# Performance work log

Hardware: AMD Instinct MI355X
Metric: run time of the kernel (lower is better)

The kernel has to match this reference:

```python
import jax, jax.numpy as jnp
import numpy as np

BS, N, D, H = 2, 512, 512, 16
DD = D // H
EPS = 1e-5


def _layernorm(h, g, b):
    mu = jnp.mean(h, axis=-1, keepdims=True)
    var = jnp.mean((h - mu) ** 2, axis=-1, keepdims=True)
    return (h - mu) / jnp.sqrt(var + EPS) * g + b


def setup_inputs() -> dict:
    key = jax.random.key(0)
    ks = jax.random.split(key, 10)
    x = jax.random.normal(ks[0], (BS, N, D), dtype=jnp.float32)
    u = jax.random.uniform(ks[1], (BS, N, N), dtype=jnp.float32)
    adj = jnp.where(u > 0.3, u, 0.0)
    s = 0.02
    return {
        "x": x,
        "adj": adj,
        "W_fc": jax.random.normal(ks[2], (D, D), dtype=jnp.float32) * s,
        "b_fc": jnp.zeros((D,), dtype=jnp.float32),
        "W_fc2": jax.random.normal(ks[3], (D, D), dtype=jnp.float32) * s,
        "b_fc2": jnp.zeros((D,), dtype=jnp.float32),
        "W_val": jax.random.normal(ks[4], (D, D), dtype=jnp.float32) * s,
        "b_val": jnp.zeros((D,), dtype=jnp.float32),
        "aff": jax.random.normal(ks[5], (H, DD), dtype=jnp.float32) * s,
        "aff_bias": jnp.zeros((H,), dtype=jnp.float32),
        "ln_g": jnp.ones((D,), dtype=jnp.float32),
        "ln_b": jnp.zeros((D,), dtype=jnp.float32),
        "t": 0,
    }


def reference(x, adj, W_fc, b_fc, W_fc2, b_fc2, W_val, b_val, aff, aff_bias, ln_g, ln_b, t):
    bs, n, d = x.shape
    # projections -> [bs, H, n, dd]
    def proj(W, b):
        return (x @ W.T + b).reshape(bs, n, H, DD).transpose(0, 2, 1, 3)
    x_val = proj(W_val, b_val)
    x_aff = proj(W_fc, b_fc)
    x_aff2 = proj(W_fc2, b_fc2)
    # GAT additive scores: leaky_relu over all (i,j) pairs, then dot with aff
    v = jax.nn.leaky_relu(x_aff[:, :, :, None, :] + x_aff2[:, :, None, :, :], 0.2)  # [bs,H,n,n,dd]
    scores = jnp.einsum('bhijd,hd->bhij', v, aff) + aff_bias[None, :, None, None]
    scores = jnp.where(adj[:, None, :, :] < 1e-5, jnp.float32(-1e9), scores)
    attn = jax.nn.softmax(scores, axis=-1)  # [bs,H,n,n]
    out = jnp.einsum('bhij,bhjd->bhid', attn, x_val)  # [bs,H,n,dd]
    out = out.transpose(0, 2, 1, 3).reshape(bs, n, d)
    x_aff_flat = x_aff.transpose(0, 2, 1, 3).reshape(bs, n, d)
    h = _layernorm(x_aff_flat + out, ln_g, ln_b)
    return jax.nn.relu(h)
```

## Files before the change

kernel.cpp:

```cpp
#include <hip/hip_runtime.h>


#define NB 2
#define NN 512
#define DM 512
#define NH 16
#define DD 32
#define RLOG2E 1.4426950408889634f

typedef __attribute__((ext_vector_type(8))) short bf16x8;
typedef __attribute__((ext_vector_type(4))) float f32x4;
typedef _Float16 h2 __attribute__((ext_vector_type(2)));
typedef __fp16 fp16x2 __attribute__((ext_vector_type(2)));

__device__ __forceinline__ h2 u2h(unsigned int u) { union { unsigned int x; h2 h; } c; c.x = u; return c.h; }
__device__ __forceinline__ unsigned int h2u(h2 v) { union { unsigned int x; h2 h; } c; c.h = v; return c.x; }
__device__ __forceinline__ h2 pkrtz(float x, float y) {
  union { fp16x2 a; h2 b; } c; c.a = __builtin_amdgcn_cvt_pkrtz(x, y); return c.b;
}

#if __has_builtin(__builtin_amdgcn_fdot2)
#define DOT2(a, b, c) __builtin_amdgcn_fdot2((a), (b), (c), false)
#else
#define DOT2(a, b, c) fmaf((float)(a)[0], (float)(b)[0], fmaf((float)(a)[1], (float)(b)[1], (c)))
#endif
#if __has_builtin(__builtin_elementwise_fma)
#define PKFMA(a, b, c) __builtin_elementwise_fma((a), (b), (c))
#else
#define PKFMA(a, b, c) ((a) * (b) + (c))
#endif

__device__ __forceinline__ unsigned short f2bf(float f) {
  unsigned int u = __float_as_uint(f);
  u = (u + 0x7FFFu + ((u >> 16) & 1u)) >> 16;
  return (unsigned short)u;
}

__global__ void prep_kernel(const float* __restrict__ x, const float* __restrict__ w0,
                            const float* __restrict__ w1, const float* __restrict__ w2,
                            const float* __restrict__ adj,
                            unsigned short* __restrict__ xb, unsigned short* __restrict__ wb0,
                            unsigned short* __restrict__ wb1, unsigned short* __restrict__ wb2,
                            unsigned int* __restrict__ bits) {
  int gid = blockIdx.x * 256 + threadIdx.x;
  if (gid < 327680) {
    const float* src; unsigned short* dst; int off;
    if (gid < 131072)      { src = x;  dst = xb;  off = gid; }
    else if (gid < 196608) { src = w0; dst = wb0; off = gid - 131072; }
    else if (gid < 262144) { src = w1; dst = wb1; off = gid - 196608; }
    else                   { src = w2; dst = wb2; off = gid - 262144; }
    float4 v = ((const float4*)src)[off];
    ushort4 r;
    r.x = f2bf(v.x); r.y = f2bf(v.y); r.z = f2bf(v.z); r.w = f2bf(v.w);
    ((ushort4*)dst)[off] = r;
  } else {
    int t = gid - 327680;
    if (t < 16384) {
      int bb = t >> 13, rem = t & 8191;
      int i = rem >> 4, jw = rem & 15;
      const float4* ap = (const float4*)(adj + ((size_t)(bb * NN + i)) * NN + jw * 32);
      unsigned int word = 0;
      #pragma unroll
      for (int q = 0; q < 8; ++q) {
        float4 v = ap[q];
        if (v.x >= 1e-5f) word |= 1u << (q * 4 + 0);
        if (v.y >= 1e-5f) word |= 1u << (q * 4 + 1);
        if (v.z >= 1e-5f) word |= 1u << (q * 4 + 2);
        if (v.w >= 1e-5f) word |= 1u << (q * 4 + 3);
      }
      bits[((bb * 16) + jw) * 512 + i] = word;
    }
  }
}

__global__ void proj_kernel(const unsigned short* __restrict__ xb,
                            const unsigned short* __restrict__ wb0,
                            const unsigned short* __restrict__ wb1,
                            const unsigned short* __restrict__ wb2,
                            const float* __restrict__ bias0, const float* __restrict__ bias1,
                            const float* __restrict__ bias2,
                            float* __restrict__ Pfc, float* __restrict__ Pfc2,
                            _Float16* __restrict__ Pfch, _Float16* __restrict__ Pfc2h,
                            _Float16* __restrict__ Pvalh) {
  const int mt = blockIdx.x, nt = blockIdx.y, which = blockIdx.z;
  const unsigned short* W = (which == 0) ? wb0 : (which == 1) ? wb1 : wb2;
  const float* bias       = (which == 0) ? bias0 : (which == 1) ? bias1 : bias2;
  float* Pf               = (which == 0) ? Pfc : (which == 1) ? Pfc2 : nullptr;
  _Float16* Ph            = (which == 0) ? Pfch : (which == 1) ? Pfc2h : Pvalh;
  const int tid = threadIdx.x;
  const int wv = tid >> 6, lane = tid & 63;
  const int wm = wv >> 1, wn = wv & 1;
  const int mbase = mt * 64 + wm * 32, nbase = nt * 64 + wn * 32;
  const int lr = lane & 15, lk = lane >> 4;
  const bf16x8* A0 = (const bf16x8*)(xb + (size_t)(mbase + lr) * 512 + lk * 8);
  const bf16x8* A1 = (const bf16x8*)(xb + (size_t)(mbase + 16 + lr) * 512 + lk * 8);
  const bf16x8* B0 = (const bf16x8*)(W + (size_t)(nbase + lr) * 512 + lk * 8);
  const bf16x8* B1 = (const bf16x8*)(W + (size_t)(nbase + 16 + lr) * 512 + lk * 8);
  f32x4 acc00 = {0.f, 0.f, 0.f, 0.f}, acc01 = acc00, acc10 = acc00, acc11 = acc00;
  #pragma unroll
  for (int kt = 0; kt < 16; ++kt) {
    bf16x8 a0 = A0[kt * 4], a1 = A1[kt * 4];
    bf16x8 b0 = B0[kt * 4], b1 = B1[kt * 4];
    acc00 = __builtin_amdgcn_mfma_f32_16x16x32_bf16(a0, b0, acc00, 0, 0, 0);
    acc01 = __builtin_amdgcn_mfma_f32_16x16x32_bf16(a0, b1, acc01, 0, 0, 0);
    acc10 = __builtin_amdgcn_mfma_f32_16x16x32_bf16(a1, b0, acc10, 0, 0, 0);
    acc11 = __builtin_amdgcn_mfma_f32_16x16x32_bf16(a1, b1, acc11, 0, 0, 0);
  }
  const int r0 = mbase + lk * 4, c0 = nbase + lr;
  #pragma unroll
  for (int v = 0; v < 4; ++v) {
    float r00 = acc00[v] + bias[c0];
    float r01 = acc01[v] + bias[c0 + 16];
    float r10 = acc10[v] + bias[c0];
    float r11 = acc11[v] + bias[c0 + 16];
    if (Pf) {
      Pf[(size_t)(r0 + v) * 512 + c0]           = r00;
      Pf[(size_t)(r0 + v) * 512 + c0 + 16]      = r01;
      Pf[(size_t)(r0 + 16 + v) * 512 + c0]      = r10;
      Pf[(size_t)(r0 + 16 + v) * 512 + c0 + 16] = r11;
    }
    Ph[(size_t)(r0 + v) * 512 + c0]           = (_Float16)r00;
    Ph[(size_t)(r0 + v) * 512 + c0 + 16]      = (_Float16)r01;
    Ph[(size_t)(r0 + 16 + v) * 512 + c0]      = (_Float16)r10;
    Ph[(size_t)(r0 + 16 + v) * 512 + c0 + 16] = (_Float16)r11;
  }
}

__global__ void aux_kernel(const float* __restrict__ Pfc, const float* __restrict__ Pfc2,
                           const float* __restrict__ aff,
                           float* __restrict__ sa, float* __restrict__ sb) {
  int gid = blockIdx.x * 256 + threadIdx.x;
  int h = gid & 15, row = gid >> 4;
  const float* ar = aff + h * 32;
  const float* p1 = Pfc + (size_t)row * 512 + h * 32;
  const float* p2 = Pfc2 + (size_t)row * 512 + h * 32;
  float s1 = 0.f, s2 = 0.f;
  #pragma unroll
  for (int d = 0; d < 32; ++d) {
    float a = ar[d];
    s1 = fmaf(a, p1[d], s1);
    s2 = fmaf(a, p2[d], s2);
  }
  int b = row >> 9, i = row & 511;
  int o = (b * NH + h) * NN + i;
  const float sc = 0.6f * RLOG2E;
  sa[o] = s1 * sc; sb[o] = s2 * sc;
}

__launch_bounds__(256)
__global__ void attn_kernel(const _Float16* __restrict__ Pfch,
                            const _Float16* __restrict__ Pfc2h,
                            const _Float16* __restrict__ Pvalh,
                            const float* __restrict__ sa, const float* __restrict__ sb,
                            const float* __restrict__ aff,
                            const unsigned int* __restrict__ bits,
                            float* __restrict__ part_l, unsigned int* __restrict__ part_o) {
  const int bx = blockIdx.x;
  const int it = bx >> 3, jh = bx & 7;
  const int h = blockIdx.y, b = blockIdx.z;
  const int tid = threadIdx.x;
  const int w = tid >> 6, lane = tid & 63;
  const int i0 = it * 128 + lane, i1 = i0 + 64;
  const int jbase = jh * 64;

  __shared__ uint4 Bt4[256];
  __shared__ uint4 Vt4[256];
  __shared__ float oacc[4096];
  __shared__ float sbt[64];
  __shared__ float slm[4][128];

  {
    const int row = tid >> 2, seg = tid & 3;
    Bt4[tid] = *(const uint4*)(Pfc2h + ((size_t)(b * NN + jbase + row)) * DM + h * DD + seg * 8);
    Vt4[tid] = *(const uint4*)(Pvalh + ((size_t)(b * NN + jbase + row)) * DM + h * DD + seg * 8);
    if (tid < 64) sbt[tid] = sb[(b * NH + h) * NN + jbase + tid];
  }

  h2 a0h[16], a1h[16], afh[16], o0h[16], o1h[16];
  {
    const uint4* ap0 = (const uint4*)(Pfch + ((size_t)(b * NN + i0)) * DM + h * DD);
    const uint4* ap1 = (const uint4*)(Pfch + ((size_t)(b * NN + i1)) * DM + h * DD);
    #pragma unroll
    for (int q = 0; q < 4; ++q) {
      uint4 v0 = ap0[q], v1 = ap1[q];
      a0h[q * 4 + 0] = u2h(v0.x); a0h[q * 4 + 1] = u2h(v0.y);
      a0h[q * 4 + 2] = u2h(v0.z); a0h[q * 4 + 3] = u2h(v0.w);
      a1h[q * 4 + 0] = u2h(v1.x); a1h[q * 4 + 1] = u2h(v1.y);
      a1h[q * 4 + 2] = u2h(v1.z); a1h[q * 4 + 3] = u2h(v1.w);
    }
    const float4* fp = (const float4*)(aff + h * DD);
    const float afs = 0.4f * RLOG2E;
    #pragma unroll
    for (int q = 0; q < 8; ++q) {
      float4 fv = fp[q];
      afh[q * 2 + 0] = pkrtz(fv.x * afs, fv.y * afs);
      afh[q * 2 + 1] = pkrtz(fv.z * afs, fv.w * afs);
    }
    #pragma unroll
    for (int k = 0; k < 16; ++k) { o0h[k] = h2{0, 0}; o1h[k] = h2{0, 0}; }
  }
  const float sai0 = sa[(b * NH + h) * NN + i0];
  const float sai1 = sa[(b * NH + h) * NN + i1];
  const unsigned int mw0 = bits[((b * 16) + jh * 2 + (w >> 1)) * NN + i0] >> ((w & 1) * 16);
  const unsigned int mw1 = bits[((b * 16) + jh * 2 + (w >> 1)) * NN + i1] >> ((w & 1) * 16);
  float l0 = 0.f, l1 = 0.f;

  __syncthreads();

  const int jt0 = w * 16;
  #pragma unroll 2
  for (int jo = 0; jo < 16; ++jo) {
    const int jl = jt0 + jo;
    uint4 bq0 = Bt4[jl * 4 + 0], bq1 = Bt4[jl * 4 + 1];
    uint4 bq2 = Bt4[jl * 4 + 2], bq3 = Bt4[jl * 4 + 3];
    const float sbj = sbt[jl];
    float t00 = 0.f, t01 = 0.f, t10 = 0.f, t11 = 0.f;
    #define SC2(k, dw, T0, T1)                                       \
      { h2 bh = u2h(dw);                                             \
        h2 u0 = u2h(h2u(a0h[k] + bh) & 0x7FFF7FFFu);                 \
        h2 u1 = u2h(h2u(a1h[k] + bh) & 0x7FFF7FFFu);                 \
        T0 = DOT2(afh[k], u0, T0);                                   \
        T1 = DOT2(afh[k], u1, T1); }
    SC2(0,  bq0.x, t00, t10) SC2(1,  bq0.y, t01, t11)
    SC2(2,  bq0.z, t00, t10) SC2(3,  bq0.w, t01, t11)
    SC2(4,  bq1.x, t00, t10) SC2(5,  bq1.y, t01, t11)
    SC2(6,  bq1.z, t00, t10) SC2(7,  bq1.w, t01, t11)
    SC2(8,  bq2.x, t00, t10) SC2(9,  bq2.y, t01, t11)
    SC2(10, bq2.z, t00, t10) SC2(11, bq2.w, t01, t11)
    SC2(12, bq3.x, t00, t10) SC2(13, bq3.y, t01, t11)
    SC2(14, bq3.z, t00, t10) SC2(15, bq3.w, t01, t11)
    #undef SC2
    const float s0 = sai0 + sbj + (t00 + t01);
    const float s1 = sai1 + sbj + (t10 + t11);
    const float bf0 = (float)((mw0 >> jo) & 1u);
    const float bf1 = (float)((mw1 >> jo) & 1u);
    const float p0 = __builtin_amdgcn_exp2f(s0) * bf0;
    const float p1 = __builtin_amdgcn_exp2f(s1) * bf1;
    l0 += p0; l1 += p1;
    const _Float16 p0s = (_Float16)p0, p1s = (_Float16)p1;
    const h2 ph0 = {p0s, p0s}, ph1 = {p1s, p1s};
    uint4 vq0 = Vt4[jl * 4 + 0], vq1 = Vt4[jl * 4 + 1];
    uint4 vq2 = Vt4[jl * 4 + 2], vq3 = Vt4[jl * 4 + 3];
    #define PVK(k, dw)                                   \
      { h2 vh = u2h(dw);                                 \
        o0h[k] = PKFMA(ph0, vh, o0h[k]);                 \
        o1h[k] = PKFMA(ph1, vh, o1h[k]); }
    PVK(0,  vq0.x) PVK(1,  vq0.y) PVK(2,  vq0.z) PVK(3,  vq0.w)
    PVK(4,  vq1.x) PVK(5,  vq1.y) PVK(6,  vq1.z) PVK(7,  vq1.w)
    PVK(8,  vq2.x) PVK(9,  vq2.y) PVK(10, vq2.z) PVK(11, vq2.w)
    PVK(12, vq3.x) PVK(13, vq3.y) PVK(14, vq3.z) PVK(15, vq3.w)
    #undef PVK
  }

  slm[w][lane] = l0; slm[w][lane + 64] = l1;

  #define MQ(Q, OP)                                                          \
    { _Pragma("unroll")                                                      \
      for (int dq = 0; dq < 8; ++dq) {                                       \
        const int d = (Q) * 8 + dq;                                          \
        const int c = (d + lane) & 31;                                       \
        OP(oacc[lane * 32 + c], (float)(o0h[d >> 1][d & 1]));                \
        OP(oacc[(lane + 64) * 32 + c], (float)(o1h[d >> 1][d & 1]));         \
      } }
  #define OPST(a, v) (a) = (v)
  #define OPAD(a, v) (a) += (v)
  __syncthreads();
  switch (w) { case 0: MQ(0, OPST) break; case 1: MQ(1, OPST) break;
               case 2: MQ(2, OPST) break; default: MQ(3, OPST) break; }
  __syncthreads();
  switch (w) { case 0: MQ(1, OPAD) break; case 1: MQ(2, OPAD) break;
               case 2: MQ(3, OPAD) break; default: MQ(0, OPAD) break; }
  __syncthreads();
  switch (w) { case 0: MQ(2, OPAD) break; case 1: MQ(3, OPAD) break;
               case 2: MQ(0, OPAD) break; default: MQ(1, OPAD) break; }
  __syncthreads();
  switch (w) { case 0: MQ(3, OPAD) break; case 1: MQ(0, OPAD) break;
               case 2: MQ(1, OPAD) break; default: MQ(2, OPAD) break; }
  __syncthreads();
  #undef MQ
  #undef OPST
  #undef OPAD

  {
    const int r = tid >> 1, hf = tid & 1;
    const size_t prow = (((size_t)(jh * 2 + b) * NH + h) * NN + it * 128 + r);
    unsigned int dws[8];
    #pragma unroll
    for (int k = 0; k < 8; ++k) {
      const int d = hf * 16 + 2 * k;
      const float v0 = oacc[r * 32 + ((d + r) & 31)];
      const float v1 = oacc[r * 32 + ((d + 1 + r) & 31)];
      dws[k] = h2u(pkrtz(v0, v1));
    }
    uint4* dst = (uint4*)(part_o + prow * 16 + hf * 8);
    dst[0] = make_uint4(dws[0], dws[1], dws[2], dws[3]);
    dst[1] = make_uint4(dws[4], dws[5], dws[6], dws[7]);
    if (hf == 0) part_l[prow] = slm[0][r] + slm[1][r] + slm[2][r] + slm[3][r];
  }
}

__global__ void comb_ln_kernel(const unsigned int* __restrict__ part_o,
                               const float* __restrict__ part_l,
                               const float* __restrict__ Pfc,
                               const float* __restrict__ g, const float* __restrict__ be,
                               float* __restrict__ out) {
  const int t = threadIdx.x;
  const int rg = blockIdx.x * 8 + (t >> 5);
  const int b = rg >> 9, i = rg & 511;
  const int l32 = t & 31;
  const int d0 = l32 * 16;
  const int h0 = d0 >> 5;
  const int dh = d0 & 31;
  float o[16];
  #pragma unroll
  for (int k = 0; k < 16; ++k) o[k] = 0.f;
  float L = 0.f;
  #pragma unroll
  for (int s = 0; s < 8; ++s) {
    const size_t prow = (((size_t)(s * 2 + b) * NH + h0) * NN + i);
    L += part_l[prow];
    const uint4* po = (const uint4*)(part_o + prow * 16 + (dh >> 1));
    uint4 q0 = po[0], q1 = po[1];
    #define ACC(k, dw) { h2 hh = u2h(dw); o[2*(k)] += (float)hh[0]; o[2*(k)+1] += (float)hh[1]; }
    ACC(0, q0.x) ACC(1, q0.y) ACC(2, q0.z) ACC(3, q0.w)
    ACC(4, q1.x) ACC(5, q1.y) ACC(6, q1.z) ACC(7, q1.w)
    #undef ACC
  }
  const float inv = 1.f / L;
  const float* pf = Pfc + ((size_t)(b * NN + i)) * DM + d0;
  float hv[16];
  float sS = 0.f, sQ = 0.f;
  #pragma unroll
  for (int k = 0; k < 4; ++k) {
    float4 pv = ((const float4*)pf)[k];
    float h0v = pv.x + o[4 * k + 0] * inv;
    float h1v = pv.y + o[4 * k + 1] * inv;
    float h2v = pv.z + o[4 * k + 2] * inv;
    float h3v = pv.w + o[4 * k + 3] * inv;
    hv[4 * k + 0] = h0v; hv[4 * k + 1] = h1v; hv[4 * k + 2] = h2v; hv[4 * k + 3] = h3v;
    sS += (h0v + h1v) + (h2v + h3v);
    sQ += (h0v * h0v + h1v * h1v) + (h2v * h2v + h3v * h3v);
  }
  #pragma unroll
  for (int off = 16; off > 0; off >>= 1) {
    sS += __shfl_xor(sS, off);
    sQ += __shfl_xor(sQ, off);
  }
  const float mu = sS * (1.f / 512.f);
  const float var = sQ * (1.f / 512.f) - mu * mu;
  const float rstd = rsqrtf(var + 1e-5f);
  float4* op = (float4*)(out + ((size_t)(b * NN + i)) * DM + d0);
  #pragma unroll
  for (int k = 0; k < 4; ++k) {
    float4 gv = ((const float4*)(g + d0))[k];
    float4 bv = ((const float4*)(be + d0))[k];
    float4 res;
    res.x = fmaxf((hv[4 * k + 0] - mu) * rstd * gv.x + bv.x, 0.f);
    res.y = fmaxf((hv[4 * k + 1] - mu) * rstd * gv.y + bv.y, 0.f);
    res.z = fmaxf((hv[4 * k + 2] - mu) * rstd * gv.z + bv.z, 0.f);
    res.w = fmaxf((hv[4 * k + 3] - mu) * rstd * gv.w + bv.w, 0.f);
    op[k] = res;
  }
}

extern "C" void kernel_launch(void* const* d_in, const int* in_sizes, int n_in,
                              void* d_out, int out_size, void* d_ws, size_t ws_size,
                              hipStream_t stream) {
  const float* x    = (const float*)d_in[0];
  const float* adj  = (const float*)d_in[1];
  const float* Wfc  = (const float*)d_in[2];
  const float* bfc  = (const float*)d_in[3];
  const float* Wfc2 = (const float*)d_in[4];
  const float* bfc2 = (const float*)d_in[5];
  const float* Wval = (const float*)d_in[6];
  const float* bval = (const float*)d_in[7];
  const float* aff  = (const float*)d_in[8];
  const float* lng  = (const float*)d_in[10];
  const float* lnb  = (const float*)d_in[11];
  float* out = (float*)d_out;

  char* ws = (char*)d_ws;
  unsigned short* xb  = (unsigned short*)(ws);
  unsigned short* wb0 = (unsigned short*)(ws + 1048576);
  unsigned short* wb1 = (unsigned short*)(ws + 1572864);
  unsigned short* wb2 = (unsigned short*)(ws + 2097152);
  unsigned int* part_o = (unsigned int*)(ws);
  float* part_l   = (float*)(ws + 8388608);
  float* Pfc      = (float*)(ws + 8912896);
  float* Pfc2     = (float*)(ws + 11010048);
  _Float16* Pfch  = (_Float16*)(ws + 13107200);
  _Float16* Pfc2h = (_Float16*)(ws + 14155776);
  _Float16* Pvalh = (_Float16*)(ws + 15204352);
  float* sa       = (float*)(ws + 16252928);
  float* sb       = (float*)(ws + 16318464);
  unsigned int* bits = (unsigned int*)(ws + 16384000);

  prep_kernel<<<1344, 256, 0, stream>>>(x, Wfc, Wfc2, Wval, adj, xb, wb0, wb1, wb2, bits);
  proj_kernel<<<dim3(16, 8, 3), 256, 0, stream>>>(xb, wb0, wb1, wb2, bfc, bfc2, bval,
                                                  Pfc, Pfc2, Pfch, Pfc2h, Pvalh);
  aux_kernel<<<64, 256, 0, stream>>>(Pfc, Pfc2, aff, sa, sb);
  attn_kernel<<<dim3(32, 16, 2), 256, 0, stream>>>(Pfch, Pfc2h, Pvalh, sa, sb, aff, bits,
                                                   part_l, part_o);
  comb_ln_kernel<<<128, 256, 0, stream>>>(part_o, part_l, Pfc, lng, lnb, out);
}
```

Measured before the change: 67.56 us.

## Compute attention P@V with fp16 MFMA via LDS and drop fp32 projection copies

```diff
diff --git a/kernel.cpp b/kernel.cpp
--- a/kernel.cpp
+++ b/kernel.cpp
@@ -11,10 +11,12 @@
 typedef __attribute__((ext_vector_type(8))) short bf16x8;
 typedef __attribute__((ext_vector_type(4))) float f32x4;
 typedef _Float16 h2 __attribute__((ext_vector_type(2)));
+typedef _Float16 h8 __attribute__((ext_vector_type(8)));
 typedef __fp16 fp16x2 __attribute__((ext_vector_type(2)));
 
 __device__ __forceinline__ h2 u2h(unsigned int u) { union { unsigned int x; h2 h; } c; c.x = u; return c.h; }
 __device__ __forceinline__ unsigned int h2u(h2 v) { union { unsigned int x; h2 h; } c; c.h = v; return c.x; }
+__device__ __forceinline__ h8 u4h8(uint4 v) { union { uint4 u; h8 h; } c; c.u = v; return c.h; }
 __device__ __forceinline__ h2 pkrtz(float x, float y) {
   union { fp16x2 a; h2 b; } c; c.a = __builtin_amdgcn_cvt_pkrtz(x, y); return c.b;
 }
@@ -23,11 +25,6 @@
 #define DOT2(a, b, c) __builtin_amdgcn_fdot2((a), (b), (c), false)
 #else
 #define DOT2(a, b, c) fmaf((float)(a)[0], (float)(b)[0], fmaf((float)(a)[1], (float)(b)[1], (c)))
-#endif
-#if __has_builtin(__builtin_elementwise_fma)
-#define PKFMA(a, b, c) __builtin_elementwise_fma((a), (b), (c))
-#else
-#define PKFMA(a, b, c) ((a) * (b) + (c))
 #endif
 
 __device__ __forceinline__ unsigned short f2bf(float f) {
@@ -79,13 +76,11 @@
                             const unsigned short* __restrict__ wb2,
                             const float* __restrict__ bias0, const float* __restrict__ bias1,
                             const float* __restrict__ bias2,
-                            float* __restrict__ Pfc, float* __restrict__ Pfc2,
                             _Float16* __restrict__ Pfch, _Float16* __restrict__ Pfc2h,
                             _Float16* __restrict__ Pvalh) {
   const int mt = blockIdx.x, nt = blockIdx.y, which = blockIdx.z;
   const unsigned short* W = (which == 0) ? wb0 : (which == 1) ? wb1 : wb2;
   const float* bias       = (which == 0) ? bias0 : (which == 1) ? bias1 : bias2;
-  float* Pf               = (which == 0) ? Pfc : (which == 1) ? Pfc2 : nullptr;
   _Float16* Ph            = (which == 0) ? Pfch : (which == 1) ? Pfc2h : Pvalh;
   const int tid = threadIdx.x;
   const int wv = tid >> 6, lane = tid & 63;
@@ -109,37 +104,28 @@
   const int r0 = mbase + lk * 4, c0 = nbase + lr;
   #pragma unroll
   for (int v = 0; v < 4; ++v) {
-    float r00 = acc00[v] + bias[c0];
-    float r01 = acc01[v] + bias[c0 + 16];
-    float r10 = acc10[v] + bias[c0];
-    float r11 = acc11[v] + bias[c0 + 16];
-    if (Pf) {
-      Pf[(size_t)(r0 + v) * 512 + c0]           = r00;
-      Pf[(size_t)(r0 + v) * 512 + c0 + 16]      = r01;
-      Pf[(size_t)(r0 + 16 + v) * 512 + c0]      = r10;
-      Pf[(size_t)(r0 + 16 + v) * 512 + c0 + 16] = r11;
-    }
-    Ph[(size_t)(r0 + v) * 512 + c0]           = (_Float16)r00;
-    Ph[(size_t)(r0 + v) * 512 + c0 + 16]      = (_Float16)r01;
-    Ph[(size_t)(r0 + 16 + v) * 512 + c0]      = (_Float16)r10;
-    Ph[(size_t)(r0 + 16 + v) * 512 + c0 + 16] = (_Float16)r11;
-  }
-}
-
-__global__ void aux_kernel(const float* __restrict__ Pfc, const float* __restrict__ Pfc2,
+    Ph[(size_t)(r0 + v) * 512 + c0]           = (_Float16)(acc00[v] + bias[c0]);
+    Ph[(size_t)(r0 + v) * 512 + c0 + 16]      = (_Float16)(acc01[v] + bias[c0 + 16]);
+    Ph[(size_t)(r0 + 16 + v) * 512 + c0]      = (_Float16)(acc10[v] + bias[c0]);
+    Ph[(size_t)(r0 + 16 + v) * 512 + c0 + 16] = (_Float16)(acc11[v] + bias[c0 + 16]);
+  }
+}
+
+__global__ void aux_kernel(const _Float16* __restrict__ Pfch, const _Float16* __restrict__ Pfc2h,
                            const float* __restrict__ aff,
                            float* __restrict__ sa, float* __restrict__ sb) {
   int gid = blockIdx.x * 256 + threadIdx.x;
   int h = gid & 15, row = gid >> 4;
   const float* ar = aff + h * 32;
-  const float* p1 = Pfc + (size_t)row * 512 + h * 32;
-  const float* p2 = Pfc2 + (size_t)row * 512 + h * 32;
+  const h2* p1 = (const h2*)(Pfch + (size_t)row * 512 + h * 32);
+  const h2* p2 = (const h2*)(Pfc2h + (size_t)row * 512 + h * 32);
   float s1 = 0.f, s2 = 0.f;
   #pragma unroll
-  for (int d = 0; d < 32; ++d) {
-    float a = ar[d];
-    s1 = fmaf(a, p1[d], s1);
-    s2 = fmaf(a, p2[d], s2);
+  for (int d2 = 0; d2 < 16; ++d2) {
+    h2 v1 = p1[d2], v2 = p2[d2];
+    float a0 = ar[2 * d2], a1 = ar[2 * d2 + 1];
+    s1 = fmaf(a0, (float)v1[0], s1); s1 = fmaf(a1, (float)v1[1], s1);
+    s2 = fmaf(a0, (float)v2[0], s2); s2 = fmaf(a1, (float)v2[1], s2);
   }
   int b = row >> 9, i = row & 511;
   int o = (b * NH + h) * NN + i;
@@ -154,7 +140,7 @@
                             const float* __restrict__ sa, const float* __restrict__ sb,
                             const float* __restrict__ aff,
                             const unsigned int* __restrict__ bits,
-                            float* __restrict__ part_l, unsigned int* __restrict__ part_o) {
+                            float* __restrict__ part_l, _Float16* __restrict__ part_oh) {
   const int bx = blockIdx.x;
   const int it = bx >> 3, jh = bx & 7;
   const int h = blockIdx.y, b = blockIdx.z;
@@ -164,19 +150,29 @@
   const int jbase = jh * 64;
 
   __shared__ uint4 Bt4[256];
-  __shared__ uint4 Vt4[256];
-  __shared__ float oacc[4096];
+  __shared__ uint4 VtT4[256];
+  __shared__ uint4 Pt4[1024];
+  __shared__ float slm[4][128];
   __shared__ float sbt[64];
-  __shared__ float slm[4][128];
 
   {
     const int row = tid >> 2, seg = tid & 3;
-    Bt4[tid] = *(const uint4*)(Pfc2h + ((size_t)(b * NN + jbase + row)) * DM + h * DD + seg * 8);
-    Vt4[tid] = *(const uint4*)(Pvalh + ((size_t)(b * NN + jbase + row)) * DM + h * DD + seg * 8);
+    uint4 bv = *(const uint4*)(Pfc2h + ((size_t)(b * NN + jbase + row)) * DM + h * DD + seg * 8);
+    Bt4[tid] = bv;
+    uint4 vv = *(const uint4*)(Pvalh + ((size_t)(b * NN + jbase + row)) * DM + h * DD + seg * 8);
+    _Float16* VtT_h = (_Float16*)VtT4;
+    const int jc = row >> 3, jr = row & 7;
+    #pragma unroll
+    for (int e = 0; e < 4; ++e) {
+      h2 pr = u2h(((const unsigned int*)&vv)[e]);
+      int d0 = seg * 8 + 2 * e, d1 = d0 + 1;
+      VtT_h[d0 * 64 + ((jc ^ (d0 & 7)) * 8) + jr] = pr[0];
+      VtT_h[d1 * 64 + ((jc ^ (d1 & 7)) * 8) + jr] = pr[1];
+    }
     if (tid < 64) sbt[tid] = sb[(b * NH + h) * NN + jbase + tid];
   }
 
-  h2 a0h[16], a1h[16], afh[16], o0h[16], o1h[16];
+  h2 a0h[16], a1h[16], afh[16];
   {
     const uint4* ap0 = (const uint4*)(Pfch + ((size_t)(b * NN + i0)) * DM + h * DD);
     const uint4* ap1 = (const uint4*)(Pfch + ((size_t)(b * NN + i1)) * DM + h * DD);
@@ -196,112 +192,104 @@
       afh[q * 2 + 0] = pkrtz(fv.x * afs, fv.y * afs);
       afh[q * 2 + 1] = pkrtz(fv.z * afs, fv.w * afs);
     }
-    #pragma unroll
-    for (int k = 0; k < 16; ++k) { o0h[k] = h2{0, 0}; o1h[k] = h2{0, 0}; }
   }
   const float sai0 = sa[(b * NH + h) * NN + i0];
   const float sai1 = sa[(b * NH + h) * NN + i1];
   const unsigned int mw0 = bits[((b * 16) + jh * 2 + (w >> 1)) * NN + i0] >> ((w & 1) * 16);
   const unsigned int mw1 = bits[((b * 16) + jh * 2 + (w >> 1)) * NN + i1] >> ((w & 1) * 16);
   float l0 = 0.f, l1 = 0.f;
+  h2 ph0[8], ph1[8];
 
   __syncthreads();
 
   const int jt0 = w * 16;
-  #pragma unroll 2
-  for (int jo = 0; jo < 16; ++jo) {
-    const int jl = jt0 + jo;
-    uint4 bq0 = Bt4[jl * 4 + 0], bq1 = Bt4[jl * 4 + 1];
-    uint4 bq2 = Bt4[jl * 4 + 2], bq3 = Bt4[jl * 4 + 3];
-    const float sbj = sbt[jl];
-    float t00 = 0.f, t01 = 0.f, t10 = 0.f, t11 = 0.f;
-    #define SC2(k, dw, T0, T1)                                       \
-      { h2 bh = u2h(dw);                                             \
-        h2 u0 = u2h(h2u(a0h[k] + bh) & 0x7FFF7FFFu);                 \
-        h2 u1 = u2h(h2u(a1h[k] + bh) & 0x7FFF7FFFu);                 \
-        T0 = DOT2(afh[k], u0, T0);                                   \
-        T1 = DOT2(afh[k], u1, T1); }
-    SC2(0,  bq0.x, t00, t10) SC2(1,  bq0.y, t01, t11)
-    SC2(2,  bq0.z, t00, t10) SC2(3,  bq0.w, t01, t11)
-    SC2(4,  bq1.x, t00, t10) SC2(5,  bq1.y, t01, t11)
-    SC2(6,  bq1.z, t00, t10) SC2(7,  bq1.w, t01, t11)
-    SC2(8,  bq2.x, t00, t10) SC2(9,  bq2.y, t01, t11)
-    SC2(10, bq2.z, t00, t10) SC2(11, bq2.w, t01, t11)
-    SC2(12, bq3.x, t00, t10) SC2(13, bq3.y, t01, t11)
-    SC2(14, bq3.z, t00, t10) SC2(15, bq3.w, t01, t11)
-    #undef SC2
-    const float s0 = sai0 + sbj + (t00 + t01);
-    const float s1 = sai1 + sbj + (t10 + t11);
-    const float bf0 = (float)((mw0 >> jo) & 1u);
-    const float bf1 = (float)((mw1 >> jo) & 1u);
-    const float p0 = __builtin_amdgcn_exp2f(s0) * bf0;
-    const float p1 = __builtin_amdgcn_exp2f(s1) * bf1;
-    l0 += p0; l1 += p1;
-    const _Float16 p0s = (_Float16)p0, p1s = (_Float16)p1;
-    const h2 ph0 = {p0s, p0s}, ph1 = {p1s, p1s};
-    uint4 vq0 = Vt4[jl * 4 + 0], vq1 = Vt4[jl * 4 + 1];
-    uint4 vq2 = Vt4[jl * 4 + 2], vq3 = Vt4[jl * 4 + 3];
-    #define PVK(k, dw)                                   \
-      { h2 vh = u2h(dw);                                 \
-        o0h[k] = PKFMA(ph0, vh, o0h[k]);                 \
-        o1h[k] = PKFMA(ph1, vh, o1h[k]); }
-    PVK(0,  vq0.x) PVK(1,  vq0.y) PVK(2,  vq0.z) PVK(3,  vq0.w)
-    PVK(4,  vq1.x) PVK(5,  vq1.y) PVK(6,  vq1.z) PVK(7,  vq1.w)
-    PVK(8,  vq2.x) PVK(9,  vq2.y) PVK(10, vq2.z) PVK(11, vq2.w)
-    PVK(12, vq3.x) PVK(13, vq3.y) PVK(14, vq3.z) PVK(15, vq3.w)
-    #undef PVK
+  #pragma unroll
+  for (int jp = 0; jp < 8; ++jp) {
+    float pe0, pe1, po0, po1;
+    #pragma unroll
+    for (int q = 0; q < 2; ++q) {
+      const int jo = jp * 2 + q;
+      const int jl = jt0 + jo;
+      uint4 bq0 = Bt4[jl * 4 + 0], bq1 = Bt4[jl * 4 + 1];
+      uint4 bq2 = Bt4[jl * 4 + 2], bq3 = Bt4[jl * 4 + 3];
+      const float sbj = sbt[jl];
+      float t00 = 0.f, t01 = 0.f, t10 = 0.f, t11 = 0.f;
+      #define SC2(k, dw, T0, T1)                                       \
+        { h2 bh = u2h(dw);                                             \
+          h2 u0 = u2h(h2u(a0h[k] + bh) & 0x7FFF7FFFu);                 \
+          h2 u1 = u2h(h2u(a1h[k] + bh) & 0x7FFF7FFFu);                 \
+          T0 = DOT2(afh[k], u0, T0);                                   \
+          T1 = DOT2(afh[k], u1, T1); }
+      SC2(0,  bq0.x, t00, t10) SC2(1,  bq0.y, t01, t11)
+      SC2(2,  bq0.z, t00, t10) SC2(3,  bq0.w, t01, t11)
+      SC2(4,  bq1.x, t00, t10) SC2(5,  bq1.y, t01, t11)
+      SC2(6,  bq1.z, t00, t10) SC2(7,  bq1.w, t01, t11)
+      SC2(8,  bq2.x, t00, t10) SC2(9,  bq2.y, t01, t11)
+      SC2(10, bq2.z, t00, t10) SC2(11, bq2.w, t01, t11)
+      SC2(12, bq3.x, t00, t10) SC2(13, bq3.y, t01, t11)
+      SC2(14, bq3.z, t00, t10) SC2(15, bq3.w, t01, t11)
+      #undef SC2
+      const float s0 = sai0 + sbj + (t00 + t01);
+      const float s1 = sai1 + sbj + (t10 + t11);
+      const float p0 = ((mw0 >> jo) & 1u) ? __builtin_amdgcn_exp2f(s0) : 0.f;
+      const float p1 = ((mw1 >> jo) & 1u) ? __builtin_amdgcn_exp2f(s1) : 0.f;
+      l0 += p0; l1 += p1;
+      if (q == 0) { pe0 = p0; pe1 = p1; } else { po0 = p0; po1 = p1; }
+    }
+    ph0[jp] = pkrtz(pe0, po0);
+    ph1[jp] = pkrtz(pe1, po1);
   }
 
   slm[w][lane] = l0; slm[w][lane + 64] = l1;
-
-  #define MQ(Q, OP)                                                          \
-    { _Pragma("unroll")                                                      \
-      for (int dq = 0; dq < 8; ++dq) {                                       \
-        const int d = (Q) * 8 + dq;                                          \
-        const int c = (d + lane) & 31;                                       \
-        OP(oacc[lane * 32 + c], (float)(o0h[d >> 1][d & 1]));                \
-        OP(oacc[(lane + 64) * 32 + c], (float)(o1h[d >> 1][d & 1]));         \
-      } }
-  #define OPST(a, v) (a) = (v)
-  #define OPAD(a, v) (a) += (v)
+  {
+    const int c0 = 2 * w, c1 = 2 * w + 1;
+    uint4 q00 = make_uint4(h2u(ph0[0]), h2u(ph0[1]), h2u(ph0[2]), h2u(ph0[3]));
+    uint4 q01 = make_uint4(h2u(ph0[4]), h2u(ph0[5]), h2u(ph0[6]), h2u(ph0[7]));
+    uint4 q10 = make_uint4(h2u(ph1[0]), h2u(ph1[1]), h2u(ph1[2]), h2u(ph1[3]));
+    uint4 q11 = make_uint4(h2u(ph1[4]), h2u(ph1[5]), h2u(ph1[6]), h2u(ph1[7]));
+    const int r0 = lane, r1 = lane + 64;
+    Pt4[r0 * 8 + (c0 ^ (r0 & 7))] = q00;
+    Pt4[r0 * 8 + (c1 ^ (r0 & 7))] = q01;
+    Pt4[r1 * 8 + (c0 ^ (r1 & 7))] = q10;
+    Pt4[r1 * 8 + (c1 ^ (r1 & 7))] = q11;
+  }
   __syncthreads();
-  switch (w) { case 0: MQ(0, OPST) break; case 1: MQ(1, OPST) break;
-               case 2: MQ(2, OPST) break; default: MQ(3, OPST) break; }
-  __syncthreads();
-  switch (w) { case 0: MQ(1, OPAD) break; case 1: MQ(2, OPAD) break;
-               case 2: MQ(3, OPAD) break; default: MQ(0, OPAD) break; }
-  __syncthreads();
-  switch (w) { case 0: MQ(2, OPAD) break; case 1: MQ(3, OPAD) break;
-               case 2: MQ(0, OPAD) break; default: MQ(1, OPAD) break; }
-  __syncthreads();
-  switch (w) { case 0: MQ(3, OPAD) break; case 1: MQ(0, OPAD) break;
-               case 2: MQ(1, OPAD) break; default: MQ(2, OPAD) break; }
-  __syncthreads();
-  #undef MQ
-  #undef OPST
-  #undef OPAD
 
   {
-    const int r = tid >> 1, hf = tid & 1;
-    const size_t prow = (((size_t)(jh * 2 + b) * NH + h) * NN + it * 128 + r);
-    unsigned int dws[8];
-    #pragma unroll
-    for (int k = 0; k < 8; ++k) {
-      const int d = hf * 16 + 2 * k;
-      const float v0 = oacc[r * 32 + ((d + r) & 31)];
-      const float v1 = oacc[r * 32 + ((d + 1 + r) & 31)];
-      dws[k] = h2u(pkrtz(v0, v1));
-    }
-    uint4* dst = (uint4*)(part_o + prow * 16 + hf * 8);
-    dst[0] = make_uint4(dws[0], dws[1], dws[2], dws[3]);
-    dst[1] = make_uint4(dws[4], dws[5], dws[6], dws[7]);
-    if (hf == 0) part_l[prow] = slm[0][r] + slm[1][r] + slm[2][r] + slm[3][r];
+    const int lr = lane & 15, lk = lane >> 4;
+    #pragma unroll
+    for (int rti = 0; rti < 2; ++rti) {
+      const int rt = w * 2 + rti;
+      const int row = rt * 16 + lr;
+      uint4 a4_0 = Pt4[row * 8 + ((lk) ^ (row & 7))];
+      uint4 a4_1 = Pt4[row * 8 + ((4 + lk) ^ (row & 7))];
+      #pragma unroll
+      for (int ct = 0; ct < 2; ++ct) {
+        const int d = ct * 16 + lr;
+        uint4 b4_0 = VtT4[d * 8 + ((lk) ^ (d & 7))];
+        uint4 b4_1 = VtT4[d * 8 + ((4 + lk) ^ (d & 7))];
+        f32x4 acc = {0.f, 0.f, 0.f, 0.f};
+        acc = __builtin_amdgcn_mfma_f32_16x16x32_f16(u4h8(a4_0), u4h8(b4_0), acc, 0, 0, 0);
+        acc = __builtin_amdgcn_mfma_f32_16x16x32_f16(u4h8(a4_1), u4h8(b4_1), acc, 0, 0, 0);
+        #pragma unroll
+        for (int v = 0; v < 4; ++v) {
+          const int grow = it * 128 + rt * 16 + lk * 4 + v;
+          const size_t prow = (((size_t)(jh * 2 + b) * NH + h) * NN + grow);
+          part_oh[prow * 32 + ct * 16 + lr] = (_Float16)acc[v];
+        }
+      }
+    }
+    if (tid < 128) {
+      const int r = tid;
+      const size_t prow = (((size_t)(jh * 2 + b) * NH + h) * NN + it * 128 + r);
+      part_l[prow] = (slm[0][r] + slm[1][r]) + (slm[2][r] + slm[3][r]);
+    }
   }
 }
 
 __global__ void comb_ln_kernel(const unsigned int* __restrict__ part_o,
                                const float* __restrict__ part_l,
-                               const float* __restrict__ Pfc,
+                               const _Float16* __restrict__ Pfch,
                                const float* __restrict__ g, const float* __restrict__ be,
                                float* __restrict__ out) {
   const int t = threadIdx.x;
@@ -327,19 +315,21 @@
     #undef ACC
   }
   const float inv = 1.f / L;
-  const float* pf = Pfc + ((size_t)(b * NN + i)) * DM + d0;
+  const uint4* pfh = (const uint4*)(Pfch + ((size_t)(b * NN + i)) * DM + d0);
+  uint4 r0 = pfh[0], r1 = pfh[1];
+  float pfv[16];
+  #define UNP(k, dw) { h2 hh = u2h(dw); pfv[2*(k)] = (float)hh[0]; pfv[2*(k)+1] = (float)hh[1]; }
+  UNP(0, r0.x) UNP(1, r0.y) UNP(2, r0.z) UNP(3, r0.w)
+  UNP(4, r1.x) UNP(5, r1.y) UNP(6, r1.z) UNP(7, r1.w)
+  #undef UNP
   float hv[16];
   float sS = 0.f, sQ = 0.f;
   #pragma unroll
-  for (int k = 0; k < 4; ++k) {
-    float4 pv = ((const float4*)pf)[k];
-    float h0v = pv.x + o[4 * k + 0] * inv;
-    float h1v = pv.y + o[4 * k + 1] * inv;
-    float h2v = pv.z + o[4 * k + 2] * inv;
-    float h3v = pv.w + o[4 * k + 3] * inv;
-    hv[4 * k + 0] = h0v; hv[4 * k + 1] = h1v; hv[4 * k + 2] = h2v; hv[4 * k + 3] = h3v;
-    sS += (h0v + h1v) + (h2v + h3v);
-    sQ += (h0v * h0v + h1v * h1v) + (h2v * h2v + h3v * h3v);
+  for (int k = 0; k < 16; ++k) {
+    float hvv = pfv[k] + o[k] * inv;
+    hv[k] = hvv;
+    sS += hvv;
+    sQ = fmaf(hvv, hvv, sQ);
   }
   #pragma unroll
   for (int off = 16; off > 0; off >>= 1) {
@@ -384,22 +374,21 @@
   unsigned short* wb0 = (unsigned short*)(ws + 1048576);
   unsigned short* wb1 = (unsigned short*)(ws + 1572864);
   unsigned short* wb2 = (unsigned short*)(ws + 2097152);
-  unsigned int* part_o = (unsigned int*)(ws);
+  _Float16* part_oh = (_Float16*)(ws);
   float* part_l   = (float*)(ws + 8388608);
-  float* Pfc      = (float*)(ws + 8912896);
-  float* Pfc2     = (float*)(ws + 11010048);
-  _Float16* Pfch  = (_Float16*)(ws + 13107200);
-  _Float16* Pfc2h = (_Float16*)(ws + 14155776);
-  _Float16* Pvalh = (_Float16*)(ws + 15204352);
-  float* sa       = (float*)(ws + 16252928);
-  float* sb       = (float*)(ws + 16318464);
-  unsigned int* bits = (unsigned int*)(ws + 16384000);
+  _Float16* Pfch  = (_Float16*)(ws + 8912896);
+  _Float16* Pfc2h = (_Float16*)(ws + 9961472);
+  _Float16* Pvalh = (_Float16*)(ws + 11010048);
+  float* sa       = (float*)(ws + 12058624);
+  float* sb       = (float*)(ws + 12124160);
+  unsigned int* bits = (unsigned int*)(ws + 12189696);
 
   prep_kernel<<<1344, 256, 0, stream>>>(x, Wfc, Wfc2, Wval, adj, xb, wb0, wb1, wb2, bits);
   proj_kernel<<<dim3(16, 8, 3), 256, 0, stream>>>(xb, wb0, wb1, wb2, bfc, bfc2, bval,
-                                                  Pfc, Pfc2, Pfch, Pfc2h, Pvalh);
-  aux_kernel<<<64, 256, 0, stream>>>(Pfc, Pfc2, aff, sa, sb);
+                                                  Pfch, Pfc2h, Pvalh);
+  aux_kernel<<<64, 256, 0, stream>>>(Pfch, Pfc2h, aff, sa, sb);
   attn_kernel<<<dim3(32, 16, 2), 256, 0, stream>>>(Pfch, Pfc2h, Pvalh, sa, sb, aff, bits,
-                                                   part_l, part_o);
-  comb_ln_kernel<<<128, 256, 0, stream>>>(part_o, part_l, Pfc, lng, lnb, out);
-}
+                                                   part_l, part_oh);
+  comb_ln_kernel<<<128, 256, 0, stream>>>((const unsigned int*)part_oh, part_l, Pfch,
+                                          lng, lnb, out);
+}
```

New measurement: 59.25 us. 12.3% less time.
